# Kernel tuning notes

Measured on AMD Instinct MI355X. Metric: run time of the kernel, lower is better.

## Reference

```python
import jax, jax.numpy as jnp
import numpy as np

N = 8192
IN_F = 256
OUT_F = 256


def setup_inputs() -> dict:
    key = jax.random.key(0)
    k1, k2, k3 = jax.random.split(key, 3)
    x = jax.random.normal(k1, (N, IN_F), dtype=jnp.float32)
    adj = jax.random.randint(k2, (N, N), 0, 2, dtype=jnp.int32)
    # glorot-uniform init over last two dims of (3, 2F, O)
    stdv = float(np.sqrt(6.0 / (2 * IN_F + OUT_F)))
    weight = jax.random.uniform(k3, (3, 2 * IN_F, OUT_F), dtype=jnp.float32,
                                minval=-stdv, maxval=stdv)
    bias = jnp.zeros((OUT_F,), dtype=jnp.float32)
    return {"g": 0, "x": x, "adj": adj, "weight": weight, "bias": bias}


def reference(g, x, adj, weight, bias):
    # per-node mean over neighbors: vectorized replacement of the python loop
    mask = (adj == 1).astype(x.dtype)               # [N, N]
    deg = jnp.sum(mask, axis=1, keepdims=True)      # [N, 1]
    x1 = (mask @ x) / deg                           # [N, F] mean aggregate
    n_x = jnp.concatenate([x1, x], axis=1)          # [N, 2F]
    # [N,2F] x [3,2F,O] broadcasts to [3,N,O]
    out = jnp.einsum('nf,kfo->kno', n_x, weight) + bias
    return out
```

## Files before the change

kernel.cpp:

```cpp
#include <hip/hip_runtime.h>


typedef unsigned short u16;
typedef int   i32x4 __attribute__((ext_vector_type(4)));
typedef unsigned u32x4 __attribute__((ext_vector_type(4)));
typedef float f32x4 __attribute__((ext_vector_type(4)));

__device__ __forceinline__ u16 f2b(float f) {
  unsigned u = __builtin_bit_cast(unsigned, f);
  return (u16)((u + 0x7FFFu + ((u >> 16) & 1u)) >> 16);
}
__device__ __forceinline__ unsigned pack2(float a, float b) {
  return (unsigned)f2b(a) | ((unsigned)f2b(b) << 16);
}
__device__ __forceinline__ f32x4 mfma16(u32x4 a, u32x4 b, f32x4 c) {
  asm("v_mfma_f32_16x16x32_bf16 %0, %1, %2, %0" : "+v"(c) : "v"(a), "v"(b));
  return c;
}

__global__ __launch_bounds__(256) void conv_xtf(const float* __restrict__ x,
                                                u16* __restrict__ xtf) {
  int c = blockIdx.x * 256 + threadIdx.x;
  int kc8 = c >> 8, f = c & 255;
  const float* p = x + (size_t)kc8 * 2048 + f;
  u32x4 h;
  h.x = pack2(p[0],    p[256]);
  h.y = pack2(p[512],  p[768]);
  h.z = pack2(p[1024], p[1280]);
  h.w = pack2(p[1536], p[1792]);
  *(u32x4*)(xtf + (size_t)c * 8) = h;
}

__global__ __launch_bounds__(256) void conv_nx(const float* __restrict__ x,
                                               u16* __restrict__ nxtf) {
  int c = blockIdx.x * 256 + threadIdx.x;
  int kc8r = c >> 13, m = c & 8191;
  const float* p = x + (size_t)m * 256 + kc8r * 8;
  f32x4 p0 = *(const f32x4*)p;
  f32x4 p1 = *(const f32x4*)(p + 4);
  u32x4 h;
  h.x = pack2(p0.x, p0.y); h.y = pack2(p0.z, p0.w);
  h.z = pack2(p1.x, p1.y); h.w = pack2(p1.z, p1.w);
  *(u32x4*)(nxtf + ((size_t)(32 + kc8r) * 8192 + m) * 8) = h;
}

__global__ __launch_bounds__(768) void conv_w(const float* __restrict__ w,
                                              u16* __restrict__ wtf) {
  int kc8 = blockIdx.x;
  int c = threadIdx.x;
  int kk = c >> 8, o = c & 255;
  const float* p = w + (size_t)kk * 131072 + (size_t)kc8 * 2048 + o;
  u32x4 h;
  h.x = pack2(p[0],    p[256]);
  h.y = pack2(p[512],  p[768]);
  h.z = pack2(p[1024], p[1280]);
  h.w = pack2(p[1536], p[1792]);
  *(u32x4*)(wtf + ((size_t)kc8 * 768 + c) * 8) = h;
}

__global__ __launch_bounds__(1024) void phase1(const int* __restrict__ adj,
                                               const u16* __restrict__ xtf,
                                               u16* __restrict__ nxtf) {
  __shared__ __align__(16) u16 AsmF[4 * 32 * 72];
  __shared__ float Csum[32 * 260];
  __shared__ int degs[1024];
  __shared__ float degrow[32];

  const int t  = threadIdx.x;
  const int g  = t >> 8;
  const int lt = t & 255;
  const int l  = t & 63;
  const int w4 = lt >> 6;
  const int l15 = l & 15, l16 = l >> 4;
  const int m0 = blockIdx.x * 32;
  const int r = lt >> 3, kq = lt & 7;

  f32x4 acc[2][4] = {};
  int dsum = 0;

  const int* arow = adj + (size_t)(m0 + r) * 8192 + g * 2048 + kq * 8;
  const int afrag0 = (g * 32 + l15) * 72 + l16 * 8;
  const u16* bbase = xtf + (size_t)l16 * 2048 + (size_t)(w4 * 64 + l15) * 8;

  for (int step = 0; step < 32; ++step) {
    const int k0 = g * 2048 + step * 64;
    __syncthreads();
    i32x4 p0 = __builtin_nontemporal_load((const i32x4*)(arow + step * 64));
    i32x4 p1 = __builtin_nontemporal_load((const i32x4*)(arow + step * 64) + 1);
    dsum += p0.x + p0.y + p0.z + p0.w + p1.x + p1.y + p1.z + p1.w;
    u32x4 h;
    h.x = (p0.x ? 0x3F80u : 0u) | (p0.y ? 0x3F800000u : 0u);
    h.y = (p0.z ? 0x3F80u : 0u) | (p0.w ? 0x3F800000u : 0u);
    h.z = (p1.x ? 0x3F80u : 0u) | (p1.y ? 0x3F800000u : 0u);
    h.w = (p1.z ? 0x3F80u : 0u) | (p1.w ? 0x3F800000u : 0u);
    *(u32x4*)&AsmF[(g * 32 + r) * 72 + kq * 8] = h;
    __syncthreads();
    const u16* bstep = bbase + ((size_t)k0 << 8);
#pragma unroll
    for (int kc = 0; kc < 2; ++kc) {
      u32x4 a0 = *(const u32x4*)&AsmF[afrag0 + kc * 32];
      u32x4 a1 = *(const u32x4*)&AsmF[afrag0 + 16 * 72 + kc * 32];
#pragma unroll
      for (int nt = 0; nt < 4; ++nt) {
        u32x4 b = *(const u32x4*)(bstep + kc * 8192 + nt * 128);
        acc[0][nt] = mfma16(a0, b, acc[0][nt]);
        acc[1][nt] = mfma16(a1, b, acc[1][nt]);
      }
    }
  }
  asm volatile("s_nop 7\n\ts_nop 7\n\ts_nop 7");

  degs[t] = dsum;
  __syncthreads();
  if (t < 32) {
    int s = 0;
#pragma unroll
    for (int gg = 0; gg < 4; ++gg)
#pragma unroll
      for (int j = 0; j < 8; ++j) s += degs[gg * 256 + t * 8 + j];
    degrow[t] = (float)s;
  }
  for (int gg = 0; gg < 4; ++gg) {
    if (g == gg) {
#pragma unroll
      for (int mt = 0; mt < 2; ++mt)
#pragma unroll
        for (int nt = 0; nt < 4; ++nt)
#pragma unroll
          for (int i = 0; i < 4; ++i) {
            int row = mt * 16 + l16 * 4 + i;
            int col = w4 * 64 + nt * 16 + l15;
            if (gg == 0) Csum[row * 260 + col] = acc[mt][nt][i];
            else         Csum[row * 260 + col] += acc[mt][nt][i];
          }
    }
    __syncthreads();
  }
  {
    int rr = t & 31, kc8 = t >> 5;
    float rd = 1.0f / degrow[rr];
    const float* cp = &Csum[rr * 260 + kc8 * 8];
    u32x4 h;
    h.x = pack2(cp[0] * rd, cp[1] * rd);
    h.y = pack2(cp[2] * rd, cp[3] * rd);
    h.z = pack2(cp[4] * rd, cp[5] * rd);
    h.w = pack2(cp[6] * rd, cp[7] * rd);
    *(u32x4*)(nxtf + ((size_t)kc8 * 8192 + m0 + rr) * 8) = h;
  }
}

__global__ __launch_bounds__(256) void phase2(const u16* __restrict__ nxtf,
                                              const u16* __restrict__ wtf,
                                              const float* __restrict__ bias,
                                              float* __restrict__ out) {
  const int t = threadIdx.x, l = t & 63, w = t >> 6;
  const int wm = w & 1, wn = w >> 1;
  const int l15 = l & 15, l16 = l >> 4;
  const int m0 = blockIdx.x * 128, c0 = blockIdx.y * 96;
  f32x4 acc[4][3] = {};
  const u16* abase = nxtf + (size_t)l16 * 65536 + (size_t)(m0 + wm * 64 + l15) * 8;
  const u16* bbase = wtf  + (size_t)l16 * 6144  + (size_t)(c0 + wn * 48 + l15) * 8;
  float bv[3];
#pragma unroll
  for (int nt = 0; nt < 3; ++nt) bv[nt] = bias[(c0 + wn * 48 + nt * 16 + l15) & 255];
#pragma unroll 2
  for (int step = 0; step < 16; ++step) {
    u32x4 a[4], b[3];
#pragma unroll
    for (int mt = 0; mt < 4; ++mt)
      a[mt] = *(const u32x4*)(abase + (size_t)step * 262144 + mt * 128);
#pragma unroll
    for (int nt = 0; nt < 3; ++nt)
      b[nt] = *(const u32x4*)(bbase + (size_t)step * 24576 + nt * 128);
#pragma unroll
    for (int mt = 0; mt < 4; ++mt)
#pragma unroll
      for (int nt = 0; nt < 3; ++nt)
        acc[mt][nt] = mfma16(a[mt], b[nt], acc[mt][nt]);
  }
  asm volatile("s_nop 7\n\ts_nop 7\n\ts_nop 7");
#pragma unroll
  for (int mt = 0; mt < 4; ++mt)
#pragma unroll
    for (int nt = 0; nt < 3; ++nt) {
      int c = c0 + wn * 48 + nt * 16 + l15;
      int kk = c >> 8, o = c & 255;
      float* op = out + (size_t)kk * 2097152 +
                  (size_t)(m0 + wm * 64 + mt * 16 + l16 * 4) * 256 + o;
#pragma unroll
      for (int i = 0; i < 4; ++i)
        __builtin_nontemporal_store(acc[mt][nt][i] + bv[nt], op + (size_t)i * 256);
    }
}

extern "C" void kernel_launch(void* const* d_in, const int* in_sizes, int n_in,
                              void* d_out, int out_size, void* d_ws, size_t ws_size,
                              hipStream_t stream) {
  (void)in_sizes; (void)n_in; (void)out_size; (void)ws_size;
  const float* x    = (const float*)d_in[1];
  const int*   adj  = (const int*)d_in[2];
  const float* wgt  = (const float*)d_in[3];
  const float* bias = (const float*)d_in[4];
  float* out = (float*)d_out;

  char* ws = (char*)d_ws;
  u16* xtf  = (u16*)ws;
  u16* nxtf = (u16*)(ws + (4u << 20));
  u16* wtf  = (u16*)(ws + (12u << 20));

  conv_xtf<<<1024, 256, 0, stream>>>(x, xtf);
  conv_nx <<<1024, 256, 0, stream>>>(x, nxtf);
  conv_w  <<<64, 768, 0, stream>>>(wgt, wtf);
  phase1  <<<256, 1024, 0, stream>>>(adj, xtf, nxtf);
  phase2  <<<dim3(64, 8), 256, 0, stream>>>(nxtf, wtf, bias, out);
}
```

Measured before the change: 433.3 us.

## Split-K phase1 across blocks with global partial reduction, merge prep kernels

The three conversion kernels are merged into one prep launch. phase1 now uses 256-thread blocks, each owning one K-quarter, so there are 1024 blocks instead of 256 blocks of 1024 threads. Each block writes fp32 partial sums and partial degrees to the workspace, and a new reducek kernel sums them, normalises and converts to bf16. phase1 also double-buffers its LDS tile and prefetches the next adjacency chunk. phase2 tiles shrink to 128x48 per block for more blocks, at the cost of about 32MB of partial-sum traffic and one extra launch.

```diff
diff --git a/kernel.cpp b/kernel.cpp
--- a/kernel.cpp
+++ b/kernel.cpp
@@ -18,93 +18,87 @@
   return c;
 }
 
-__global__ __launch_bounds__(256) void conv_xtf(const float* __restrict__ x,
-                                                u16* __restrict__ xtf) {
-  int c = blockIdx.x * 256 + threadIdx.x;
-  int kc8 = c >> 8, f = c & 255;
-  const float* p = x + (size_t)kc8 * 2048 + f;
-  u32x4 h;
-  h.x = pack2(p[0],    p[256]);
-  h.y = pack2(p[512],  p[768]);
-  h.z = pack2(p[1024], p[1280]);
-  h.w = pack2(p[1536], p[1792]);
-  *(u32x4*)(xtf + (size_t)c * 8) = h;
-}
-
-__global__ __launch_bounds__(256) void conv_nx(const float* __restrict__ x,
-                                               u16* __restrict__ nxtf) {
-  int c = blockIdx.x * 256 + threadIdx.x;
-  int kc8r = c >> 13, m = c & 8191;
-  const float* p = x + (size_t)m * 256 + kc8r * 8;
-  f32x4 p0 = *(const f32x4*)p;
-  f32x4 p1 = *(const f32x4*)(p + 4);
-  u32x4 h;
-  h.x = pack2(p0.x, p0.y); h.y = pack2(p0.z, p0.w);
-  h.z = pack2(p1.x, p1.y); h.w = pack2(p1.z, p1.w);
-  *(u32x4*)(nxtf + ((size_t)(32 + kc8r) * 8192 + m) * 8) = h;
-}
-
-__global__ __launch_bounds__(768) void conv_w(const float* __restrict__ w,
-                                              u16* __restrict__ wtf) {
-  int kc8 = blockIdx.x;
-  int c = threadIdx.x;
-  int kk = c >> 8, o = c & 255;
-  const float* p = w + (size_t)kk * 131072 + (size_t)kc8 * 2048 + o;
-  u32x4 h;
-  h.x = pack2(p[0],    p[256]);
-  h.y = pack2(p[512],  p[768]);
-  h.z = pack2(p[1024], p[1280]);
-  h.w = pack2(p[1536], p[1792]);
-  *(u32x4*)(wtf + ((size_t)kc8 * 768 + c) * 8) = h;
-}
-
-__global__ __launch_bounds__(1024) void phase1(const int* __restrict__ adj,
-                                               const u16* __restrict__ xtf,
-                                               u16* __restrict__ nxtf) {
-  __shared__ __align__(16) u16 AsmF[4 * 32 * 72];
-  __shared__ float Csum[32 * 260];
-  __shared__ int degs[1024];
-  __shared__ float degrow[32];
-
-  const int t  = threadIdx.x;
-  const int g  = t >> 8;
-  const int lt = t & 255;
-  const int l  = t & 63;
-  const int w4 = lt >> 6;
+__global__ __launch_bounds__(256) void prep(const float* __restrict__ x,
+                                            const float* __restrict__ wgt,
+                                            u16* __restrict__ xtf,
+                                            u16* __restrict__ nxtf,
+                                            u16* __restrict__ wtf) {
+  const int b = blockIdx.x, t = threadIdx.x;
+  if (b < 1024) {
+    int c = b * 256 + t, kc8 = c >> 8, f = c & 255;
+    const float* p = x + (size_t)kc8 * 2048 + f;
+    u32x4 h;
+    h.x = pack2(p[0],    p[256]);  h.y = pack2(p[512],  p[768]);
+    h.z = pack2(p[1024], p[1280]); h.w = pack2(p[1536], p[1792]);
+    *(u32x4*)(xtf + (size_t)c * 8) = h;
+  } else if (b < 2048) {
+    int c = (b - 1024) * 256 + t, kc8r = c >> 13, m = c & 8191;
+    const float* p = x + (size_t)m * 256 + kc8r * 8;
+    f32x4 p0 = *(const f32x4*)p, p1 = *(const f32x4*)(p + 4);
+    u32x4 h;
+    h.x = pack2(p0.x, p0.y); h.y = pack2(p0.z, p0.w);
+    h.z = pack2(p1.x, p1.y); h.w = pack2(p1.z, p1.w);
+    *(u32x4*)(nxtf + ((size_t)(32 + kc8r) * 8192 + m) * 8) = h;
+  } else {
+    int idx = b - 2048, kc8 = idx / 3, c = (idx % 3) * 256 + t;
+    int kk = c >> 8, o = c & 255;
+    const float* p = wgt + (size_t)kk * 131072 + (size_t)kc8 * 2048 + o;
+    u32x4 h;
+    h.x = pack2(p[0],    p[256]);  h.y = pack2(p[512],  p[768]);
+    h.z = pack2(p[1024], p[1280]); h.w = pack2(p[1536], p[1792]);
+    *(u32x4*)(wtf + ((size_t)kc8 * 768 + c) * 8) = h;
+  }
+}
+
+__global__ __launch_bounds__(256) void phase1(const int* __restrict__ adj,
+                                              const u16* __restrict__ xtf,
+                                              float* __restrict__ part,
+                                              int* __restrict__ degp) {
+  __shared__ __align__(16) u16 As[2][32 * 72];
+  __shared__ int degs[256];
+
+  const int t = threadIdx.x, l = t & 63, w = t >> 6;
   const int l15 = l & 15, l16 = l >> 4;
-  const int m0 = blockIdx.x * 32;
-  const int r = lt >> 3, kq = lt & 7;
+  const int g = blockIdx.x & 3, mt = blockIdx.x >> 2;
+  const int m0 = mt * 32, k0g = g * 2048;
+  const int r = t >> 3, kq = t & 7;
 
   f32x4 acc[2][4] = {};
   int dsum = 0;
 
-  const int* arow = adj + (size_t)(m0 + r) * 8192 + g * 2048 + kq * 8;
-  const int afrag0 = (g * 32 + l15) * 72 + l16 * 8;
-  const u16* bbase = xtf + (size_t)l16 * 2048 + (size_t)(w4 * 64 + l15) * 8;
+  const i32x4* arow = (const i32x4*)(adj + (size_t)(m0 + r) * 8192 + k0g) + kq * 2;
+  const int lds_w  = r * 72 + kq * 8;
+  const int lds_a0 = l15 * 72 + l16 * 8;
+  const int lds_a1 = lds_a0 + 16 * 72;
+  const u16* bbase = xtf + ((size_t)(k0g >> 3) + l16) * 2048 + (size_t)(w * 64 + l15) * 8;
+
+  i32x4 p0 = __builtin_nontemporal_load(arow);
+  i32x4 p1 = __builtin_nontemporal_load(arow + 1);
 
   for (int step = 0; step < 32; ++step) {
-    const int k0 = g * 2048 + step * 64;
-    __syncthreads();
-    i32x4 p0 = __builtin_nontemporal_load((const i32x4*)(arow + step * 64));
-    i32x4 p1 = __builtin_nontemporal_load((const i32x4*)(arow + step * 64) + 1);
     dsum += p0.x + p0.y + p0.z + p0.w + p1.x + p1.y + p1.z + p1.w;
     u32x4 h;
     h.x = (p0.x ? 0x3F80u : 0u) | (p0.y ? 0x3F800000u : 0u);
     h.y = (p0.z ? 0x3F80u : 0u) | (p0.w ? 0x3F800000u : 0u);
     h.z = (p1.x ? 0x3F80u : 0u) | (p1.y ? 0x3F800000u : 0u);
     h.w = (p1.z ? 0x3F80u : 0u) | (p1.w ? 0x3F800000u : 0u);
-    *(u32x4*)&AsmF[(g * 32 + r) * 72 + kq * 8] = h;
+    *(u32x4*)&As[step & 1][lds_w] = h;
+    if (step < 31) {
+      p0 = __builtin_nontemporal_load(arow + (step + 1) * 16);
+      p1 = __builtin_nontemporal_load(arow + (step + 1) * 16 + 1);
+    }
     __syncthreads();
-    const u16* bstep = bbase + ((size_t)k0 << 8);
+    const u16* bs = bbase + (size_t)step * 16384;
+    const u16* as_ = &As[step & 1][0];
 #pragma unroll
     for (int kc = 0; kc < 2; ++kc) {
-      u32x4 a0 = *(const u32x4*)&AsmF[afrag0 + kc * 32];
-      u32x4 a1 = *(const u32x4*)&AsmF[afrag0 + 16 * 72 + kc * 32];
+      u32x4 a0 = *(const u32x4*)(as_ + lds_a0 + kc * 32);
+      u32x4 a1 = *(const u32x4*)(as_ + lds_a1 + kc * 32);
 #pragma unroll
       for (int nt = 0; nt < 4; ++nt) {
-        u32x4 b = *(const u32x4*)(bstep + kc * 8192 + nt * 128);
-        acc[0][nt] = mfma16(a0, b, acc[0][nt]);
-        acc[1][nt] = mfma16(a1, b, acc[1][nt]);
+        u32x4 bfr = *(const u32x4*)(bs + (size_t)kc * 8192 + nt * 128);
+        acc[0][nt] = mfma16(a0, bfr, acc[0][nt]);
+        acc[1][nt] = mfma16(a1, bfr, acc[1][nt]);
       }
     }
   }
@@ -115,38 +109,38 @@
   if (t < 32) {
     int s = 0;
 #pragma unroll
-    for (int gg = 0; gg < 4; ++gg)
-#pragma unroll
-      for (int j = 0; j < 8; ++j) s += degs[gg * 256 + t * 8 + j];
-    degrow[t] = (float)s;
-  }
+    for (int j = 0; j < 8; ++j) s += degs[t * 8 + j];
+    degp[g * 8192 + m0 + t] = s;
+  }
+  float* pc = part + ((size_t)g * 8192 + m0) * 256;
+#pragma unroll
+  for (int mt2 = 0; mt2 < 2; ++mt2)
+#pragma unroll
+    for (int nt = 0; nt < 4; ++nt)
+#pragma unroll
+      for (int i = 0; i < 4; ++i)
+        pc[(size_t)(mt2 * 16 + l16 * 4 + i) * 256 + (w * 64 + nt * 16 + l15)] =
+            acc[mt2][nt][i];
+}
+
+__global__ __launch_bounds__(256) void reducek(const float* __restrict__ part,
+                                               const int* __restrict__ degp,
+                                               u16* __restrict__ nxtf) {
+  int c = blockIdx.x * 256 + threadIdx.x;
+  int m = c >> 5, kc8 = c & 31;
+  int deg = degp[m] + degp[8192 + m] + degp[16384 + m] + degp[24576 + m];
+  float rd = 1.0f / (float)deg;
+  const float* p = part + (size_t)m * 256 + kc8 * 8;
+  f32x4 s0 = {}, s1 = {};
+#pragma unroll
   for (int gg = 0; gg < 4; ++gg) {
-    if (g == gg) {
-#pragma unroll
-      for (int mt = 0; mt < 2; ++mt)
-#pragma unroll
-        for (int nt = 0; nt < 4; ++nt)
-#pragma unroll
-          for (int i = 0; i < 4; ++i) {
-            int row = mt * 16 + l16 * 4 + i;
-            int col = w4 * 64 + nt * 16 + l15;
-            if (gg == 0) Csum[row * 260 + col] = acc[mt][nt][i];
-            else         Csum[row * 260 + col] += acc[mt][nt][i];
-          }
-    }
-    __syncthreads();
-  }
-  {
-    int rr = t & 31, kc8 = t >> 5;
-    float rd = 1.0f / degrow[rr];
-    const float* cp = &Csum[rr * 260 + kc8 * 8];
-    u32x4 h;
-    h.x = pack2(cp[0] * rd, cp[1] * rd);
-    h.y = pack2(cp[2] * rd, cp[3] * rd);
-    h.z = pack2(cp[4] * rd, cp[5] * rd);
-    h.w = pack2(cp[6] * rd, cp[7] * rd);
-    *(u32x4*)(nxtf + ((size_t)kc8 * 8192 + m0 + rr) * 8) = h;
-  }
+    s0 += *(const f32x4*)(p + (size_t)gg * 2097152);
+    s1 += *(const f32x4*)(p + (size_t)gg * 2097152 + 4);
+  }
+  u32x4 h;
+  h.x = pack2(s0.x * rd, s0.y * rd); h.y = pack2(s0.z * rd, s0.w * rd);
+  h.z = pack2(s1.x * rd, s1.y * rd); h.w = pack2(s1.z * rd, s1.w * rd);
+  *(u32x4*)(nxtf + ((size_t)kc8 * 8192 + m) * 8) = h;
 }
 
 __global__ __launch_bounds__(256) void phase2(const u16* __restrict__ nxtf,
@@ -154,42 +148,40 @@
                                               const float* __restrict__ bias,
                                               float* __restrict__ out) {
   const int t = threadIdx.x, l = t & 63, w = t >> 6;
-  const int wm = w & 1, wn = w >> 1;
   const int l15 = l & 15, l16 = l >> 4;
-  const int m0 = blockIdx.x * 128, c0 = blockIdx.y * 96;
-  f32x4 acc[4][3] = {};
-  const u16* abase = nxtf + (size_t)l16 * 65536 + (size_t)(m0 + wm * 64 + l15) * 8;
-  const u16* bbase = wtf  + (size_t)l16 * 6144  + (size_t)(c0 + wn * 48 + l15) * 8;
+  const int m0 = blockIdx.x * 128, c0 = blockIdx.y * 48;
+  f32x4 acc[2][3] = {};
+  const u16* abase = nxtf + (size_t)l16 * 65536 + (size_t)(m0 + w * 32 + l15) * 8;
+  const u16* bbase = wtf  + (size_t)l16 * 6144  + (size_t)(c0 + l15) * 8;
   float bv[3];
 #pragma unroll
-  for (int nt = 0; nt < 3; ++nt) bv[nt] = bias[(c0 + wn * 48 + nt * 16 + l15) & 255];
+  for (int nt = 0; nt < 3; ++nt) bv[nt] = bias[(c0 + nt * 16 + l15) & 255];
 #pragma unroll 2
   for (int step = 0; step < 16; ++step) {
-    u32x4 a[4], b[3];
-#pragma unroll
-    for (int mt = 0; mt < 4; ++mt)
-      a[mt] = *(const u32x4*)(abase + (size_t)step * 262144 + mt * 128);
+    u32x4 a[2], b[3];
+    a[0] = *(const u32x4*)(abase + (size_t)step * 262144);
+    a[1] = *(const u32x4*)(abase + (size_t)step * 262144 + 128);
 #pragma unroll
     for (int nt = 0; nt < 3; ++nt)
       b[nt] = *(const u32x4*)(bbase + (size_t)step * 24576 + nt * 128);
 #pragma unroll
-    for (int mt = 0; mt < 4; ++mt)
+    for (int mt2 = 0; mt2 < 2; ++mt2)
 #pragma unroll
       for (int nt = 0; nt < 3; ++nt)
-        acc[mt][nt] = mfma16(a[mt], b[nt], acc[mt][nt]);
+        acc[mt2][nt] = mfma16(a[mt2], b[nt], acc[mt2][nt]);
   }
   asm volatile("s_nop 7\n\ts_nop 7\n\ts_nop 7");
 #pragma unroll
-  for (int mt = 0; mt < 4; ++mt)
+  for (int mt2 = 0; mt2 < 2; ++mt2)
 #pragma unroll
     for (int nt = 0; nt < 3; ++nt) {
-      int c = c0 + wn * 48 + nt * 16 + l15;
+      int c = c0 + nt * 16 + l15;
       int kk = c >> 8, o = c & 255;
       float* op = out + (size_t)kk * 2097152 +
-                  (size_t)(m0 + wm * 64 + mt * 16 + l16 * 4) * 256 + o;
+                  (size_t)(m0 + w * 32 + mt2 * 16 + l16 * 4) * 256 + o;
 #pragma unroll
       for (int i = 0; i < 4; ++i)
-        __builtin_nontemporal_store(acc[mt][nt][i] + bv[nt], op + (size_t)i * 256);
+        __builtin_nontemporal_store(acc[mt2][nt][i] + bv[nt], op + (size_t)i * 256);
     }
 }
 
@@ -204,13 +196,14 @@
   float* out = (float*)d_out;
 
   char* ws = (char*)d_ws;
-  u16* xtf  = (u16*)ws;
-  u16* nxtf = (u16*)(ws + (4u << 20));
-  u16* wtf  = (u16*)(ws + (12u << 20));
-
-  conv_xtf<<<1024, 256, 0, stream>>>(x, xtf);
-  conv_nx <<<1024, 256, 0, stream>>>(x, nxtf);
-  conv_w  <<<64, 768, 0, stream>>>(wgt, wtf);
-  phase1  <<<256, 1024, 0, stream>>>(adj, xtf, nxtf);
-  phase2  <<<dim3(64, 8), 256, 0, stream>>>(nxtf, wtf, bias, out);
-}
+  u16*   xtf  = (u16*)ws;
+  u16*   nxtf = (u16*)(ws + (4ull  << 20));
+  u16*   wtf  = (u16*)(ws + (12ull << 20));
+  float* part = (float*)(ws + (13ull << 20));
+  int*   degp = (int*)(ws + (45ull << 20));
+
+  prep   <<<2240, 256, 0, stream>>>(x, wgt, xtf, nxtf, wtf);
+  phase1 <<<1024, 256, 0, stream>>>(adj, xtf, part, degp);
+  reducek<<<1024, 256, 0, stream>>>(part, degp, nxtf);
+  phase2 <<<dim3(64, 16), 256, 0, stream>>>(nxtf, wtf, bias, out);
+}
```

New measurement: 435.6 us. About the same (+0.5%).
